# Optimization experiments

Hardware: AMD Instinct MI355X
Metric: run time of the kernel (lower is better)

The kernel has to match this reference:

```python
import jax, jax.numpy as jnp
import numpy as np

B, S, D, H, P = 4, 2048, 1024, 16, 10
DK = D // H

def setup_inputs() -> dict:
    key = jax.random.key(0)
    ks = jax.random.split(key, 12)
    inp = {
        'q': jax.random.normal(ks[0], (B, S, D), jnp.float32),
        'k': jax.random.normal(ks[1], (B, S, D), jnp.float32),
        'v': jax.random.normal(ks[2], (B, S, D), jnp.float32),
        # causal mask, broadcastable over batch/heads
        'mask': jnp.tril(jnp.ones((S, S), jnp.int32))[None, None, :, :],
        'Wq': jax.random.normal(ks[3], (D, D), jnp.float32) * (1.0 / np.sqrt(D)),
        'bq': jnp.zeros((D,), jnp.float32),
        'Wk': jax.random.normal(ks[4], (D, D), jnp.float32) * (1.0 / np.sqrt(D)),
        'bk': jnp.zeros((D,), jnp.float32),
        'Wv': jax.random.normal(ks[5], (D, D), jnp.float32) * (1.0 / np.sqrt(D)),
        'bv': jnp.zeros((D,), jnp.float32),
        'Wo': jax.random.normal(ks[6], (D, D), jnp.float32) * (1.0 / np.sqrt(D)),
        'bo': jnp.zeros((D,), jnp.float32),
        'prefix_k': jax.random.normal(ks[7], (H, P, DK), jnp.float32) * 0.02,
        'prefix_v': jax.random.normal(ks[8], (H, P, DK), jnp.float32) * 0.02,
    }
    return inp

def reference(q, k, v, mask, Wq, bq, Wk, bk, Wv, bv, Wo, bo, prefix_k, prefix_v):
    bs, sq, d = q.shape
    h, p, dk = prefix_k.shape
    # projections -> [B, H, S, dk]
    Q = (q @ Wq + bq).reshape(bs, sq, h, dk).transpose(0, 2, 1, 3)
    K = (k @ Wk + bk).reshape(bs, -1, h, dk).transpose(0, 2, 1, 3)
    V = (v @ Wv + bv).reshape(bs, -1, h, dk).transpose(0, 2, 1, 3)
    # prepend learnable prefix K/V along the key axis
    pK = jnp.broadcast_to(prefix_k[None], (bs, h, p, dk))
    pV = jnp.broadcast_to(prefix_v[None], (bs, h, p, dk))
    K = jnp.concatenate([pK, K], axis=2)  # [B,H,P+S,dk]
    V = jnp.concatenate([pV, V], axis=2)
    # extend mask: prefix positions always visible
    pref_mask = jnp.ones(mask.shape[:3] + (p,), mask.dtype)
    full_mask = jnp.concatenate([pref_mask, mask], axis=-1)  # [.,.,S,P+S]
    scores = jnp.einsum('bhqd,bhkd->bhqk', Q, K) / np.sqrt(dk).astype(jnp.float32)
    scores = jnp.where(full_mask == 0, jnp.asarray(-1e9, scores.dtype), scores)
    attn = jax.nn.softmax(scores, axis=-1)  # dropout in eval mode: identity
    out = jnp.einsum('bhqk,bhkd->bhqd', attn, V)
    out = out.transpose(0, 2, 1, 3).reshape(bs, sq, d)
    return out @ Wo + bo
```

## Files before the change

### kernel.cpp

```cpp
#include <hip/hip_runtime.h>

typedef __bf16 bf16x8 __attribute__((ext_vector_type(8)));
typedef __bf16 bf16x4 __attribute__((ext_vector_type(4)));
typedef float f32x4 __attribute__((ext_vector_type(4)));

constexpr int Sq = 2048, Dd = 1024, Hn = 16, Pn = 10, DK = 64;
constexpr int SKPAD = 2112;
constexpr int NBH = 64;
constexpr float LOG2E = 1.44269504088896340736f;

__device__ __forceinline__ float exp2_fast(float x) {
  return __builtin_amdgcn_exp2f(x);
}

__device__ __forceinline__ unsigned short f2bf(float f) {
  unsigned int u = __float_as_uint(f);
  u += 0x7fffu + ((u >> 16) & 1u);
  return (unsigned short)(u >> 16);
}

__device__ __forceinline__ void gload_lds16(const void* g, void* l) {
  __builtin_amdgcn_global_load_lds(
      (const __attribute__((address_space(1))) void*)g,
      (__attribute__((address_space(3))) void*)l, 16, 0, 0);
}

__device__ __forceinline__ f32x4 mfma16(bf16x8 a, bf16x8 b, f32x4 c) {
  return __builtin_amdgcn_mfma_f32_16x16x32_bf16(a, b, c, 0, 0, 0);
}

__global__ void k_cvt3(const float* __restrict__ i0, const float* __restrict__ i1,
                       const float* __restrict__ i2, unsigned short* __restrict__ o0,
                       unsigned short* __restrict__ o1, unsigned short* __restrict__ o2,
                       int n4) {
  const float* in; unsigned short* out;
  switch (blockIdx.y) {
    case 0: in = i0; out = o0; break;
    case 1: in = i1; out = o1; break;
    default: in = i2; out = o2; break;
  }
  int i = blockIdx.x * blockDim.x + threadIdx.x;
  int st = gridDim.x * blockDim.x;
  for (; i < n4; i += st) {
    float4 v = reinterpret_cast<const float4*>(in)[i];
    ushort4 r;
    r.x = f2bf(v.x); r.y = f2bf(v.y); r.z = f2bf(v.z); r.w = f2bf(v.w);
    reinterpret_cast<ushort4*>(out)[i] = r;
  }
}

__global__ void k_wt(const float* __restrict__ W0, const float* __restrict__ W1,
                     const float* __restrict__ W2, const float* __restrict__ W3,
                     unsigned short* __restrict__ T0, unsigned short* __restrict__ T1,
                     unsigned short* __restrict__ T2, unsigned short* __restrict__ T3) {
  __shared__ float tile[32][33];
  const float* W; unsigned short* T;
  switch (blockIdx.z) {
    case 0: W = W0; T = T0; break;
    case 1: W = W1; T = T1; break;
    case 2: W = W2; T = T2; break;
    default: W = W3; T = T3; break;
  }
  int n0 = blockIdx.x * 32, k0 = blockIdx.y * 32;
  int tx = threadIdx.x, ty = threadIdx.y;
  for (int r = ty; r < 32; r += 8)
    tile[r][tx] = W[(size_t)(k0 + r) * Dd + n0 + tx];
  __syncthreads();
  for (int r = ty; r < 32; r += 8)
    T[(size_t)(n0 + r) * Dd + k0 + tx] = f2bf(tile[tx][r]);
}

__global__ void k_fill(const float* __restrict__ pk, const float* __restrict__ pv,
                       unsigned short* __restrict__ Kb, unsigned short* __restrict__ Vt) {
  int bh = blockIdx.x;
  int h = bh & (Hn - 1);
  unsigned short* Kbh = Kb + (size_t)bh * SKPAD * DK;
  unsigned short* Vth = Vt + (size_t)bh * DK * SKPAD;
  for (int i = threadIdx.x; i < Pn * DK; i += blockDim.x) {
    int p = i >> 6, dk = i & 63;
    float kv = pk[((size_t)h * Pn + p) * DK + dk];
    float vv = pv[((size_t)h * Pn + p) * DK + dk];
    Kbh[(Sq + p) * DK + dk] = f2bf(kv);
    Vth[(size_t)dk * SKPAD + Sq + p] = f2bf(vv);
  }
  constexpr int ZR = SKPAD - (Pn + Sq);
  for (int i = threadIdx.x; i < ZR * DK; i += blockDim.x) {
    int r = i >> 6, c = i & 63;
    Kbh[(Sq + Pn + r) * DK + c] = 0;
    Vth[(size_t)c * SKPAD + (Sq + Pn + r)] = 0;
  }
}

__global__ __launch_bounds__(256, 4) void k_gemm_qkv(
    const unsigned short* __restrict__ Aq, const unsigned short* __restrict__ Ak,
    const unsigned short* __restrict__ Av,
    const unsigned short* __restrict__ Wq, const unsigned short* __restrict__ Wk,
    const unsigned short* __restrict__ Wv,
    const float* __restrict__ bq, const float* __restrict__ bk,
    const float* __restrict__ bv,
    unsigned short* __restrict__ Qo, unsigned short* __restrict__ Ko,
    unsigned short* __restrict__ Vo, float qscale) {
  __shared__ unsigned short S[2 * 128 * 64];
  unsigned short* As = S;
  unsigned short* Bs = S + 128 * 64;
  int bx0 = blockIdx.x;
  int orig = (bx0 & 7) * 192 + (bx0 >> 3);
  int stream = orig >> 9, within = orig & 511;

  const unsigned short *A, *Bt; const float* bias;
  unsigned short* outB; float scale;
  switch (stream) {
    case 0:  A = Aq; Bt = Wq; bias = bq; outB = Qo; scale = qscale; break;
    case 1:  A = Ak; Bt = Wk; bias = bk; outB = Ko; scale = 1.f; break;
    default: A = Av; Bt = Wv; bias = bv; outB = Vo; scale = 1.f; break;
  }

  int tid = threadIdx.x;
  int w = tid >> 6, l = tid & 63;
  int lq = l & 15, lg = l >> 4;
  int tm = within >> 3, tn = within & 7;
  int brow = tm * 128, bcol = tn * 128;
  int wm = w >> 1, wn = w & 1;

  f32x4 acc[4][4];
#pragma unroll
  for (int m = 0; m < 4; ++m)
#pragma unroll
    for (int n = 0; n < 4; ++n) acc[m][n] = (f32x4){0.f, 0.f, 0.f, 0.f};

  for (int kt = 0; kt < 1024; kt += 64) {
#pragma unroll
    for (int it = 0; it < 4; ++it) {
      int c = it * 256 + tid;
      int row = c >> 3, col = c & 7;
      gload_lds16(A + (size_t)(brow + row) * 1024 + kt + col * 8,
                  As + (size_t)(it * 256 + w * 64) * 8);
      gload_lds16(Bt + (size_t)(bcol + row) * 1024 + kt + col * 8,
                  Bs + (size_t)(it * 256 + w * 64) * 8);
    }
    asm volatile("s_waitcnt vmcnt(0)" ::: "memory");
    __syncthreads();
    const bf16x8* As8 = reinterpret_cast<const bf16x8*>(As);
    const bf16x8* Bs8 = reinterpret_cast<const bf16x8*>(Bs);
#pragma unroll
    for (int ks = 0; ks < 2; ++ks) {
      bf16x8 af[4], bfv[4];
#pragma unroll
      for (int m = 0; m < 4; ++m)
        af[m] = As8[(size_t)(wm * 64 + m * 16 + lq) * 8 + ks * 4 + lg];
#pragma unroll
      for (int n = 0; n < 4; ++n)
        bfv[n] = Bs8[(size_t)(wn * 64 + n * 16 + lq) * 8 + ks * 4 + lg];
#pragma unroll
      for (int m = 0; m < 4; ++m)
#pragma unroll
        for (int n = 0; n < 4; ++n)
          acc[m][n] = mfma16(af[m], bfv[n], acc[m][n]);
    }
    __syncthreads();
  }

  if (stream < 2) {
#pragma unroll
    for (int n = 0; n < 4; ++n) {
      int N = bcol + wn * 64 + n * 16 + lq;
      float bv = bias[N];
#pragma unroll
      for (int m = 0; m < 4; ++m) {
        int M0 = brow + wm * 64 + m * 16 + lg * 4;
#pragma unroll
        for (int r = 0; r < 4; ++r) {
          float val = (acc[m][n][r] + bv) * scale;
          int Mr = M0 + r;
          int b = Mr >> 11, s = Mr & 2047;
          int h = N >> 6, dk = N & 63;
          size_t idx;
          if (stream == 0) idx = (((size_t)(b * Hn + h)) * Sq + s) * DK + dk;
          else             idx = (((size_t)(b * Hn + h)) * SKPAD + s) * DK + dk;
          outB[idx] = f2bf(val);
        }
      }
    }
  } else {
    __syncthreads();
    unsigned short* T = S;
#pragma unroll
    for (int n = 0; n < 4; ++n) {
      int col = wn * 64 + n * 16 + lq;
      float bv = bias[bcol + col];
      int sw = (col & 7) << 4;
#pragma unroll
      for (int m = 0; m < 4; ++m) {
        int row0 = wm * 64 + m * 16 + lg * 4;
        ushort4 p4;
        p4.x = f2bf(acc[m][n][0] + bv);
        p4.y = f2bf(acc[m][n][1] + bv);
        p4.z = f2bf(acc[m][n][2] + bv);
        p4.w = f2bf(acc[m][n][3] + bv);
        *reinterpret_cast<ushort4*>(&T[col * 128 + (row0 ^ sw)]) = p4;
      }
    }
    __syncthreads();
    int b = brow >> 11, s0 = brow & 2047;
    int col = tid >> 1;
    int off = (tid & 1) * 64;
    int sw = (col & 7) << 4;
    int h = (bcol + col) >> 6, dk = (bcol + col) & 63;
    unsigned short* dst = Vo + (((size_t)(b * Hn + h)) * DK + dk) * SKPAD + s0 + off;
#pragma unroll
    for (int j = 0; j < 8; ++j) {
      int4 v = *reinterpret_cast<const int4*>(&T[col * 128 + ((off + j * 8) ^ sw)]);
      *reinterpret_cast<int4*>(dst + j * 8) = v;
    }
  }
}

__global__ __launch_bounds__(256, 4) void k_gemm_o(
    const unsigned short* __restrict__ A, const unsigned short* __restrict__ Bt,
    const float* __restrict__ bias, float* __restrict__ outF) {
  __shared__ unsigned short As[128 * 64];
  __shared__ unsigned short Bs[128 * 64];
  int bx0 = blockIdx.x;
  int within = (bx0 & 7) * 64 + (bx0 >> 3);
  int tid = threadIdx.x;
  int w = tid >> 6, l = tid & 63;
  int lq = l & 15, lg = l >> 4;
  int tm = within >> 3, tn = within & 7;
  int brow = tm * 128, bcol = tn * 128;
  int wm = w >> 1, wn = w & 1;

  f32x4 acc[4][4];
#pragma unroll
  for (int m = 0; m < 4; ++m)
#pragma unroll
    for (int n = 0; n < 4; ++n) acc[m][n] = (f32x4){0.f, 0.f, 0.f, 0.f};

  for (int kt = 0; kt < 1024; kt += 64) {
#pragma unroll
    for (int it = 0; it < 4; ++it) {
      int c = it * 256 + tid;
      int row = c >> 3, col = c & 7;
      gload_lds16(A + (size_t)(brow + row) * 1024 + kt + col * 8,
                  As + (size_t)(it * 256 + w * 64) * 8);
      gload_lds16(Bt + (size_t)(bcol + row) * 1024 + kt + col * 8,
                  Bs + (size_t)(it * 256 + w * 64) * 8);
    }
    asm volatile("s_waitcnt vmcnt(0)" ::: "memory");
    __syncthreads();
    const bf16x8* As8 = reinterpret_cast<const bf16x8*>(As);
    const bf16x8* Bs8 = reinterpret_cast<const bf16x8*>(Bs);
#pragma unroll
    for (int ks = 0; ks < 2; ++ks) {
      bf16x8 af[4], bfv[4];
#pragma unroll
      for (int m = 0; m < 4; ++m)
        af[m] = As8[(size_t)(wm * 64 + m * 16 + lq) * 8 + ks * 4 + lg];
#pragma unroll
      for (int n = 0; n < 4; ++n)
        bfv[n] = Bs8[(size_t)(wn * 64 + n * 16 + lq) * 8 + ks * 4 + lg];
#pragma unroll
      for (int m = 0; m < 4; ++m)
#pragma unroll
        for (int n = 0; n < 4; ++n)
          acc[m][n] = mfma16(af[m], bfv[n], acc[m][n]);
    }
    __syncthreads();
  }

#pragma unroll
  for (int n = 0; n < 4; ++n) {
    int N = bcol + wn * 64 + n * 16 + lq;
    float bv = bias[N];
#pragma unroll
    for (int m = 0; m < 4; ++m) {
      int M0 = brow + wm * 64 + m * 16 + lg * 4;
#pragma unroll
      for (int r = 0; r < 4; ++r)
        outF[(size_t)(M0 + r) * 1024 + N] = acc[m][n][r] + bv;
    }
  }
}

__global__ __launch_bounds__(256, 4) void k_attn(
    const unsigned short* __restrict__ Qb, const unsigned short* __restrict__ Kb,
    const unsigned short* __restrict__ Vt, unsigned short* __restrict__ O) {
  __shared__ unsigned short Ks[2][64 * 64];
  __shared__ unsigned short Vs[2][64 * 64];
  __shared__ unsigned short Ps[4][16 * 64];
  int tid = threadIdx.x;
  int w = tid >> 6, l = tid & 63;
  int lq = l & 15, lg = l >> 4;
  int bh = blockIdx.x;
  int pi = blockIdx.y;
  int qtL = pi, qtH = 31 - pi;
  int ntot = qtH + 2;
  int qsA[2] = {qtL * 64, qtH * 64};

  bf16x8 qf[2][2];
#pragma unroll
  for (int qt = 0; qt < 2; ++qt) {
    const unsigned short* Qg = Qb + ((size_t)bh * Sq + qsA[qt] + w * 16) * DK;
#pragma unroll
    for (int ks = 0; ks < 2; ++ks)
      qf[qt][ks] = *reinterpret_cast<const bf16x8*>(
          Qg + (size_t)lq * DK + ks * 32 + lg * 8);
  }

  const unsigned short* Kg = Kb + (size_t)bh * SKPAD * DK;
  const unsigned short* Vg = Vt + (size_t)bh * DK * SKPAD;

  float m_run[2] = {-1e30f, -1e30f};
  float l_part[2] = {0.f, 0.f};
  f32x4 oacc[2][4];
#pragma unroll
  for (int qt = 0; qt < 2; ++qt)
#pragma unroll
    for (int n = 0; n < 4; ++n) oacc[qt][n] = (f32x4){0.f, 0.f, 0.f, 0.f};

  unsigned short* Pw = &Ps[w][0];

  auto STAGE = [&](int b, int tile) {
    int kt = tile * 64;
#pragma unroll
    for (int it = 0; it < 2; ++it) {
      int dst = (it * 256 + tid) * 16;
      int srcK = dst ^ (((dst >> 7) & 7) << 4);
      gload_lds16((const char*)(Kg + (size_t)kt * DK) + srcK,
                  (char*)Ks[b] + (size_t)(it * 256 + w * 64) * 16);
    }
#pragma unroll
    for (int it = 0; it < 2; ++it) {
      int dst = (it * 256 + tid) * 16;
      int row = dst >> 7;
      int colb = (dst & 127) ^ ((row & 7) << 4);
      gload_lds16((const char*)(Vg + (size_t)row * SKPAD + kt) + colb,
                  (char*)Vs[b] + (size_t)(it * 256 + w * 64) * 16);
    }
  };

  STAGE(0, 0);
  asm volatile("s_waitcnt vmcnt(0)" ::: "memory");
  __syncthreads();

  for (int t = 0; t < ntot; ++t) {
    int bsel = t & 1;
    bool isLast = (t == ntot - 1);
    if (!isLast) STAGE(bsel ^ 1, (t + 1 == ntot - 1) ? (Sq / 64) : (t + 1));
    int kt = isLast ? Sq : t * 64;

#pragma unroll
    for (int qt = 0; qt < 2; ++qt) {
      int qs = qsA[qt];
      if (!isLast) {
        if (qt == 0 && t > qtL) continue;
        if (kt > qs + w * 16 + 15) continue;
      }

      f32x4 st[4];
#pragma unroll
      for (int m = 0; m < 4; ++m) st[m] = (f32x4){0.f, 0.f, 0.f, 0.f};
      __builtin_amdgcn_s_setprio(1);
#pragma unroll
      for (int ks = 0; ks < 2; ++ks) {
#pragma unroll
        for (int m = 0; m < 4; ++m) {
          if (isLast && m > 0) continue;
          int krow = m * 16 + lq;
          int byt = (krow * 128 + ks * 64 + lg * 16) ^ ((krow & 7) << 4);
          bf16x8 kf = *reinterpret_cast<const bf16x8*>((const char*)Ks[bsel] + byt);
          st[m] = mfma16(kf, qf[qt][ks], st[m]);
        }
      }
      __builtin_amdgcn_s_setprio(0);

      if (isLast) {
#pragma unroll
        for (int m = 0; m < 4; ++m)
#pragma unroll
          for (int r = 0; r < 4; ++r) {
            int ki = m * 16 + lg * 4 + r;
            st[m][r] = (ki < Pn) ? st[m][r] : -1e30f;
          }
      } else if (kt + 63 > qs + w * 16) {
        int qrow = qs + w * 16 + lq;
#pragma unroll
        for (int m = 0; m < 4; ++m)
#pragma unroll
          for (int r = 0; r < 4; ++r) {
            int key = kt + m * 16 + lg * 4 + r;
            st[m][r] = (key <= qrow) ? st[m][r] : -1e30f;
          }
      }

      float mx = fmaxf(fmaxf(st[0][0], st[0][1]), fmaxf(st[0][2], st[0][3]));
#pragma unroll
      for (int m = 1; m < 4; ++m)
        mx = fmaxf(mx, fmaxf(fmaxf(st[m][0], st[m][1]), fmaxf(st[m][2], st[m][3])));
      if (__any(mx > m_run[qt] + 8.f)) {
        float gmx = fmaxf(mx, __shfl_xor(mx, 16));
        gmx = fmaxf(gmx, __shfl_xor(gmx, 32));
        float mnew = fmaxf(m_run[qt], gmx);
        float alpha = exp2_fast(m_run[qt] - mnew);
        m_run[qt] = mnew;
        l_part[qt] *= alpha;
        float ar[4];
#pragma unroll
        for (int r = 0; r < 4; ++r) ar[r] = __shfl(alpha, lg * 4 + r);
#pragma unroll
        for (int n = 0; n < 4; ++n)
#pragma unroll
          for (int r = 0; r < 4; ++r) oacc[qt][n][r] *= ar[r];
      }
      float rs = 0.f;
#pragma unroll
      for (int m = 0; m < 4; ++m) {
        bf16x4 p4;
#pragma unroll
        for (int r = 0; r < 4; ++r) {
          float p = exp2_fast(st[m][r] - m_run[qt]);
          rs += p;
          p4[r] = (__bf16)p;
        }
        int byt = (lq * 128 + m * 32 + lg * 8) ^ ((lq & 7) << 4);
        *reinterpret_cast<bf16x4*>((char*)Pw + byt) = p4;
      }
      l_part[qt] += rs;

      __builtin_amdgcn_s_setprio(1);
#pragma unroll
      for (int ks = 0; ks < 2; ++ks) {
        if (isLast && ks == 1) continue;
        int pbyt = (lq * 128 + ks * 64 + lg * 16) ^ ((lq & 7) << 4);
        bf16x8 pf = *reinterpret_cast<const bf16x8*>((const char*)Pw + pbyt);
#pragma unroll
        for (int n = 0; n < 4; ++n) {
          int dv = n * 16 + lq;
          int vbyt = (dv * 128 + ks * 64 + lg * 16) ^ ((dv & 7) << 4);
          bf16x8 vf = *reinterpret_cast<const bf16x8*>((const char*)Vs[bsel] + vbyt);
          oacc[qt][n] = mfma16(pf, vf, oacc[qt][n]);
        }
      }
      __builtin_amdgcn_s_setprio(0);
    }
    asm volatile("s_waitcnt vmcnt(0)" ::: "memory");
    __syncthreads();
  }

  int b = bh >> 4, h = bh & 15;
#pragma unroll
  for (int qt = 0; qt < 2; ++qt) {
    float ls = l_part[qt];
    ls += __shfl_xor(ls, 16);
    ls += __shfl_xor(ls, 32);
    float lr[4];
#pragma unroll
    for (int r = 0; r < 4; ++r) lr[r] = 1.0f / __shfl(ls, lg * 4 + r);
#pragma unroll
    for (int n = 0; n < 4; ++n)
#pragma unroll
      for (int r = 0; r < 4; ++r) {
        int qrow2 = qsA[qt] + w * 16 + lg * 4 + r;
        size_t idx = ((size_t)b * Sq + qrow2) * Dd + h * DK + n * 16 + lq;
        O[idx] = f2bf(oacc[qt][n][r] * lr[r]);
      }
  }
}

extern "C" void kernel_launch(void* const* d_in, const int* in_sizes, int n_in,
                              void* d_out, int out_size, void* d_ws, size_t ws_size,
                              hipStream_t stream) {
  (void)in_sizes; (void)n_in; (void)out_size; (void)ws_size;
  const float* q  = (const float*)d_in[0];
  const float* k  = (const float*)d_in[1];
  const float* v  = (const float*)d_in[2];
  const float* Wq = (const float*)d_in[4];
  const float* bq = (const float*)d_in[5];
  const float* Wk = (const float*)d_in[6];
  const float* bk = (const float*)d_in[7];
  const float* Wv = (const float*)d_in[8];
  const float* bv = (const float*)d_in[9];
  const float* Wo = (const float*)d_in[10];
  const float* bo = (const float*)d_in[11];
  const float* pk = (const float*)d_in[12];
  const float* pv = (const float*)d_in[13];

  unsigned short* wsp = (unsigned short*)d_ws;
  size_t off = 0;
  auto take = [&](size_t elems) { unsigned short* p = wsp + off; off += elems; return p; };
  unsigned short* qc  = take(8388608);
  unsigned short* kc  = take(8388608);
  unsigned short* vc  = take(8388608);
  unsigned short* wqt = take(1048576);
  unsigned short* wkt = take(1048576);
  unsigned short* wvt = take(1048576);
  unsigned short* wot = take(1048576);
  unsigned short* Qbf = take(8388608);
  unsigned short* KbB = take((size_t)NBH * SKPAD * DK);
  unsigned short* VtB = take((size_t)NBH * DK * SKPAD);
  unsigned short* Ob  = qc;
  float* outF = (float*)d_out;

  k_cvt3<<<dim3(1024, 3), 256, 0, stream>>>(q, k, v, qc, kc, vc, 8388608 / 4);
  k_wt<<<dim3(32, 32, 4), dim3(32, 8), 0, stream>>>(Wq, Wk, Wv, Wo, wqt, wkt, wvt, wot);
  k_fill<<<64, 256, 0, stream>>>(pk, pv, KbB, VtB);
  k_gemm_qkv<<<1536, 256, 0, stream>>>(qc, kc, vc, wqt, wkt, wvt,
                                       bq, bk, bv, Qbf, KbB, VtB,
                                       0.125f * LOG2E);
  k_attn<<<dim3(NBH, 16), 256, 0, stream>>>(Qbf, KbB, VtB, Ob);
  k_gemm_o<<<512, 256, 0, stream>>>(Ob, wot, bo, outF);
}
```

Measured before the change: 203.8 us.

## Fuse fp32-to-bf16 input conversion into QKV GEMM with swizzled LDS tiles

Removes the separate conversion kernel that turned q, k and v from fp32 into bf16. The QKV GEMM now loads fp32 activation tiles straight into LDS and converts them to bf16 when reading MFMA fragments. It also adds an XOR swizzle to both the A and B LDS layouts to reduce bank conflicts. In exchange, the A tile uses twice the LDS and global load traffic per k-step, and occupancy drops from 4 to 3 blocks per CU.

Measured after the change: 185.7 us. 8.9% less time.

```diff
diff --git a/kernel.cpp b/kernel.cpp
--- a/kernel.cpp
+++ b/kernel.cpp
@@ -27,26 +27,6 @@
 
 __device__ __forceinline__ f32x4 mfma16(bf16x8 a, bf16x8 b, f32x4 c) {
   return __builtin_amdgcn_mfma_f32_16x16x32_bf16(a, b, c, 0, 0, 0);
-}
-
-__global__ void k_cvt3(const float* __restrict__ i0, const float* __restrict__ i1,
-                       const float* __restrict__ i2, unsigned short* __restrict__ o0,
-                       unsigned short* __restrict__ o1, unsigned short* __restrict__ o2,
-                       int n4) {
-  const float* in; unsigned short* out;
-  switch (blockIdx.y) {
-    case 0: in = i0; out = o0; break;
-    case 1: in = i1; out = o1; break;
-    default: in = i2; out = o2; break;
-  }
-  int i = blockIdx.x * blockDim.x + threadIdx.x;
-  int st = gridDim.x * blockDim.x;
-  for (; i < n4; i += st) {
-    float4 v = reinterpret_cast<const float4*>(in)[i];
-    ushort4 r;
-    r.x = f2bf(v.x); r.y = f2bf(v.y); r.z = f2bf(v.z); r.w = f2bf(v.w);
-    reinterpret_cast<ushort4*>(out)[i] = r;
-  }
 }
 
 __global__ void k_wt(const float* __restrict__ W0, const float* __restrict__ W1,
@@ -91,28 +71,27 @@
   }
 }
 
-__global__ __launch_bounds__(256, 4) void k_gemm_qkv(
-    const unsigned short* __restrict__ Aq, const unsigned short* __restrict__ Ak,
-    const unsigned short* __restrict__ Av,
+__global__ __launch_bounds__(256, 3) void k_gemm_qkv(
+    const float* __restrict__ Aq, const float* __restrict__ Ak,
+    const float* __restrict__ Av,
     const unsigned short* __restrict__ Wq, const unsigned short* __restrict__ Wk,
     const unsigned short* __restrict__ Wv,
     const float* __restrict__ bq, const float* __restrict__ bk,
     const float* __restrict__ bv,
     unsigned short* __restrict__ Qo, unsigned short* __restrict__ Ko,
     unsigned short* __restrict__ Vo, float qscale) {
-  __shared__ unsigned short S[2 * 128 * 64];
-  unsigned short* As = S;
-  unsigned short* Bs = S + 128 * 64;
+  __shared__ float Af[128 * 64];
+  __shared__ unsigned short Bs[128 * 64];
   int bx0 = blockIdx.x;
   int orig = (bx0 & 7) * 192 + (bx0 >> 3);
   int stream = orig >> 9, within = orig & 511;
 
-  const unsigned short *A, *Bt; const float* bias;
+  const float* A32; const unsigned short* Bt; const float* bias;
   unsigned short* outB; float scale;
   switch (stream) {
-    case 0:  A = Aq; Bt = Wq; bias = bq; outB = Qo; scale = qscale; break;
-    case 1:  A = Ak; Bt = Wk; bias = bk; outB = Ko; scale = 1.f; break;
-    default: A = Av; Bt = Wv; bias = bv; outB = Vo; scale = 1.f; break;
+    case 0:  A32 = Aq; Bt = Wq; bias = bq; outB = Qo; scale = qscale; break;
+    case 1:  A32 = Ak; Bt = Wk; bias = bk; outB = Ko; scale = 1.f; break;
+    default: A32 = Av; Bt = Wv; bias = bv; outB = Vo; scale = 1.f; break;
   }
 
   int tid = threadIdx.x;
@@ -130,27 +109,48 @@
 
   for (int kt = 0; kt < 1024; kt += 64) {
 #pragma unroll
+    for (int it = 0; it < 8; ++it) {
+      int c = it * 256 + tid;
+      int row = c >> 4;
+      int cb = (c & 15) * 16;
+      int sb = cb ^ ((row & 7) << 4);
+      gload_lds16((const char*)(A32 + (size_t)(brow + row) * 1024 + kt) + sb,
+                  (char*)Af + (size_t)(it * 256 + w * 64) * 16);
+    }
+#pragma unroll
     for (int it = 0; it < 4; ++it) {
       int c = it * 256 + tid;
-      int row = c >> 3, col = c & 7;
-      gload_lds16(A + (size_t)(brow + row) * 1024 + kt + col * 8,
-                  As + (size_t)(it * 256 + w * 64) * 8);
-      gload_lds16(Bt + (size_t)(bcol + row) * 1024 + kt + col * 8,
-                  Bs + (size_t)(it * 256 + w * 64) * 8);
+      int row = c >> 3;
+      int cb = (c & 7) * 16;
+      int sb = cb ^ ((row & 7) << 4);
+      gload_lds16((const char*)(Bt + (size_t)(bcol + row) * 1024 + kt) + sb,
+                  (char*)Bs + (size_t)(it * 256 + w * 64) * 16);
     }
     asm volatile("s_waitcnt vmcnt(0)" ::: "memory");
     __syncthreads();
-    const bf16x8* As8 = reinterpret_cast<const bf16x8*>(As);
-    const bf16x8* Bs8 = reinterpret_cast<const bf16x8*>(Bs);
 #pragma unroll
     for (int ks = 0; ks < 2; ++ks) {
       bf16x8 af[4], bfv[4];
 #pragma unroll
-      for (int m = 0; m < 4; ++m)
-        af[m] = As8[(size_t)(wm * 64 + m * 16 + lq) * 8 + ks * 4 + lg];
-#pragma unroll
-      for (int n = 0; n < 4; ++n)
-        bfv[n] = Bs8[(size_t)(wn * 64 + n * 16 + lq) * 8 + ks * 4 + lg];
+      for (int m = 0; m < 4; ++m) {
+        int row = wm * 64 + m * 16 + lq;
+        int b0 = row * 256 + ks * 128 + lg * 32;
+        int sw = (row & 7) << 4;
+        f32x4 a0 = *reinterpret_cast<const f32x4*>((const char*)Af + (b0 ^ sw));
+        f32x4 a1 = *reinterpret_cast<const f32x4*>((const char*)Af + ((b0 + 16) ^ sw));
+        bf16x8 v;
+        v[0] = (__bf16)a0[0]; v[1] = (__bf16)a0[1];
+        v[2] = (__bf16)a0[2]; v[3] = (__bf16)a0[3];
+        v[4] = (__bf16)a1[0]; v[5] = (__bf16)a1[1];
+        v[6] = (__bf16)a1[2]; v[7] = (__bf16)a1[3];
+        af[m] = v;
+      }
+#pragma unroll
+      for (int n = 0; n < 4; ++n) {
+        int row = wn * 64 + n * 16 + lq;
+        int byt = (row * 128 + ks * 64 + lg * 16) ^ ((row & 7) << 4);
+        bfv[n] = *reinterpret_cast<const bf16x8*>((const char*)Bs + byt);
+      }
 #pragma unroll
       for (int m = 0; m < 4; ++m)
 #pragma unroll
@@ -183,7 +183,7 @@
     }
   } else {
     __syncthreads();
-    unsigned short* T = S;
+    unsigned short* T = (unsigned short*)Af;
 #pragma unroll
     for (int n = 0; n < 4; ++n) {
       int col = wn * 64 + n * 16 + lq;
@@ -487,9 +487,7 @@
   unsigned short* wsp = (unsigned short*)d_ws;
   size_t off = 0;
   auto take = [&](size_t elems) { unsigned short* p = wsp + off; off += elems; return p; };
-  unsigned short* qc  = take(8388608);
-  unsigned short* kc  = take(8388608);
-  unsigned short* vc  = take(8388608);
+  unsigned short* Ob  = take(8388608);
   unsigned short* wqt = take(1048576);
   unsigned short* wkt = take(1048576);
   unsigned short* wvt = take(1048576);
@@ -497,13 +495,11 @@
   unsigned short* Qbf = take(8388608);
   unsigned short* KbB = take((size_t)NBH * SKPAD * DK);
   unsigned short* VtB = take((size_t)NBH * DK * SKPAD);
-  unsigned short* Ob  = qc;
   float* outF = (float*)d_out;
 
-  k_cvt3<<<dim3(1024, 3), 256, 0, stream>>>(q, k, v, qc, kc, vc, 8388608 / 4);
   k_wt<<<dim3(32, 32, 4), dim3(32, 8), 0, stream>>>(Wq, Wk, Wv, Wo, wqt, wkt, wvt, wot);
   k_fill<<<64, 256, 0, stream>>>(pk, pv, KbB, VtB);
-  k_gemm_qkv<<<1536, 256, 0, stream>>>(qc, kc, vc, wqt, wkt, wvt,
+  k_gemm_qkv<<<1536, 256, 0, stream>>>(q, k, v, wqt, wkt, wvt,
                                        bq, bk, bv, Qbf, KbB, VtB,
                                        0.125f * LOG2E);
   k_attn<<<dim3(NBH, 16), 256, 0, stream>>>(Qbf, KbB, VtB, Ob);
```
